# Kernel optimization log

Hardware: AMD Instinct MI355X
Metric: run time of the kernel (lower is better)

Reference implementation:

```python
import jax, jax.numpy as jnp
import numpy as np

N_NODES = 150000  # n_users + m_items
NUM_LAYERS = 3


def setup_inputs() -> dict:
    key = jax.random.key(0)
    k1, k2 = jax.random.split(key)
    x = jax.random.normal(k1, (N_NODES, 64), dtype=jnp.float32) * 0.1
    edge_index = jax.random.randint(k2, (2, 4800000), 0, N_NODES, dtype=jnp.int64)
    return {"x": x, "edge_index": edge_index}


def _lightgcn_propagate(x, row, col, deg_inv_sqrt):
    # message: norm * x[row], aggregated into col (sum)
    norm = deg_inv_sqrt[row] * deg_inv_sqrt[col]  # [E]
    msg = x[row] * norm[:, None]                   # [E, D]
    return jax.ops.segment_sum(msg, col, num_segments=x.shape[0])


def reference(x, edge_index):
    row, col = edge_index[0], edge_index[1]
    # symmetric GCN normalization: deg from destination nodes
    ones = jnp.ones(row.shape, dtype=x.dtype)
    deg = jax.ops.segment_sum(ones, col, num_segments=x.shape[0])
    deg_inv_sqrt = jnp.where(deg > 0, jax.lax.rsqrt(jnp.maximum(deg, 1.0)), 0.0)

    alpha = 1.0 / (1.0 + NUM_LAYERS)
    out = jnp.zeros_like(x)
    h = x
    for _ in range(NUM_LAYERS):
        h = _lightgcn_propagate(h, row, col, deg_inv_sqrt)
        out = out + alpha * h
    return out
```

## Files before the change

### kernel.cpp

```cpp
#include <hip/hip_runtime.h>
#include <hip/hip_fp16.h>
#include <math.h>

#define N_NODES 150000
#define D 64
#define NEDGE 4800000
#define NUM_LAYERS 3

#define BSHIFT 8
#define NBUCKET ((N_NODES + 255) >> 8)
#define NBPAD 768
#define BINTILE 8192
#define NBIN_BLOCKS ((NEDGE + BINTILE - 1) / BINTILE)
#define SCAP 9216

typedef float v2f __attribute__((ext_vector_type(2)));

__global__ void hist_bucket(const int4* __restrict__ col4, int* __restrict__ bcount) {
    __shared__ int h[NBUCKET];
    for (int i = threadIdx.x; i < NBUCKET; i += blockDim.x) h[i] = 0;
    __syncthreads();
    int i = blockIdx.x * blockDim.x + threadIdx.x;
    int stride = gridDim.x * blockDim.x;
    for (int e = i; e < NEDGE / 4; e += stride) {
        int4 c = col4[e];
        atomicAdd(&h[c.x >> BSHIFT], 1);
        atomicAdd(&h[c.y >> BSHIFT], 1);
        atomicAdd(&h[c.z >> BSHIFT], 1);
        atomicAdd(&h[c.w >> BSHIFT], 1);
    }
    __syncthreads();
    for (int b = threadIdx.x; b < NBUCKET; b += blockDim.x)
        if (h[b]) atomicAdd(&bcount[b], h[b]);
}

__global__ void scan_buckets(const int* __restrict__ bcount, int* __restrict__ bbase,
                             int* __restrict__ bcur16, int* __restrict__ off) {
    __shared__ int tsum[256];
    int t = threadIdx.x;
    int loc[3];
    int s = 0;
#pragma unroll
    for (int k = 0; k < 3; k++) {
        int idx = t * 3 + k;
        int x = (idx < NBUCKET) ? bcount[idx] : 0;
        loc[k] = x;
        s += x;
    }
    tsum[t] = s;
    __syncthreads();
    for (int ofs = 1; ofs < 256; ofs <<= 1) {
        int xv = (t >= ofs) ? tsum[t - ofs] : 0;
        __syncthreads();
        tsum[t] += xv;
        __syncthreads();
    }
    int run = (t > 0) ? tsum[t - 1] : 0;
#pragma unroll
    for (int k = 0; k < 3; k++) {
        int idx = t * 3 + k;
        if (idx < NBUCKET) bbase[idx] = run;
        bcur16[idx * 16] = run;
        run += loc[k];
    }
    if (t == 255) {
        bbase[NBUCKET] = NEDGE;
        off[N_NODES] = NEDGE;
    }
}

__global__ void __launch_bounds__(256) binpass2(const int* __restrict__ row,
                                                const int* __restrict__ col,
                                                int* __restrict__ bcur16,
                                                unsigned* __restrict__ bin) {
    __shared__ unsigned srec[BINTILE];
    __shared__ int hist[NBPAD];
    __shared__ int lscan[NBPAD];
    __shared__ int lcur[NBPAD];
    __shared__ int gbase[NBPAD];
    __shared__ int tsum[256];
    int t = threadIdx.x;
    int base = blockIdx.x * BINTILE;
    int n = NEDGE - base;
    if (n > BINTILE) n = BINTILE;
    for (int i = t; i < NBPAD; i += 256) hist[i] = 0;
    __syncthreads();
    for (int i = t; i < n; i += 256)
        atomicAdd(&hist[col[base + i] >> BSHIFT], 1);
    __syncthreads();
    int b0 = t * 3;
    int l0 = hist[b0], l1 = hist[b0 + 1], l2 = hist[b0 + 2];
    tsum[t] = l0 + l1 + l2;
    __syncthreads();
    for (int ofs = 1; ofs < 256; ofs <<= 1) {
        int xv = (t >= ofs) ? tsum[t - ofs] : 0;
        __syncthreads();
        tsum[t] += xv;
        __syncthreads();
    }
    int run = (t > 0) ? tsum[t - 1] : 0;
    lscan[b0] = run; lcur[b0] = run;
    lscan[b0 + 1] = run + l0; lcur[b0 + 1] = run + l0;
    lscan[b0 + 2] = run + l0 + l1; lcur[b0 + 2] = run + l0 + l1;
    gbase[b0]     = l0 ? atomicAdd(&bcur16[b0 * 16], l0) : 0;
    gbase[b0 + 1] = l1 ? atomicAdd(&bcur16[(b0 + 1) * 16], l1) : 0;
    gbase[b0 + 2] = l2 ? atomicAdd(&bcur16[(b0 + 2) * 16], l2) : 0;
    __syncthreads();
    for (int i = t; i < n; i += 256) {
        int c = col[base + i];
        int r = row[base + i];
        int b = c >> BSHIFT;
        int pos = atomicAdd(&lcur[b], 1);
        srec[pos] = (unsigned)r | ((unsigned)(c & 255) << 18);
    }
    __syncthreads();
#pragma unroll
    for (int k = 0; k < 3; k++) {
        int b = b0 + k;
        int s = lscan[b], e2 = lcur[b], gb = gbase[b];
        for (int j = s; j < e2; j++) bin[gb + (j - s)] = srec[j];
    }
}

__global__ void __launch_bounds__(256) sortpass2(const unsigned* __restrict__ bin,
                                                 const int* __restrict__ bbase,
                                                 float* __restrict__ dis,
                                                 int* __restrict__ off,
                                                 unsigned* __restrict__ ewf) {
    __shared__ unsigned srec[SCAP];
    __shared__ int hist[256];
    __shared__ int sc[256];
    __shared__ int ncur[256];
    int b = blockIdx.x, t = threadIdx.x;
    int s = bbase[b], e = bbase[b + 1];
    int len = e - s;
    int nst = len < SCAP ? len : SCAP;
    for (int i = t; i < nst; i += 256) srec[i] = bin[s + i];
    hist[t] = 0;
    __syncthreads();
    for (int i = t; i < nst; i += 256)
        atomicAdd(&hist[srec[i] >> 18], 1);
    for (int i = nst + t; i < len; i += 256)
        atomicAdd(&hist[bin[s + i] >> 18], 1);
    __syncthreads();
    int val = hist[t];
    sc[t] = val;
    __syncthreads();
    for (int ofs = 1; ofs < 256; ofs <<= 1) {
        int xv = (t >= ofs) ? sc[t - ofs] : 0;
        __syncthreads();
        sc[t] += xv;
        __syncthreads();
    }
    int ex = sc[t] - val;
    ncur[t] = ex;
    int node = (b << BSHIFT) + t;
    if (node < N_NODES) {
        dis[node] = (val > 0) ? (1.0f / sqrtf((float)val)) : 0.0f;
        off[node] = s + ex;
    }
    __syncthreads();
#pragma unroll
    for (int q = 0; q < 5; q++) {
        for (int i = t; i < nst; i += 256) {
            unsigned rec = srec[i];
            unsigned src = rec & 0x3FFFFu;
            if ((src >> 15) == (unsigned)q) {
                int c = (int)(rec >> 18);
                int pos = s + atomicAdd(&ncur[c], 1);
                ewf[pos] = src;
            }
        }
        __syncthreads();
    }
    for (int i = nst + t; i < len; i += 256) {
        unsigned rec = bin[s + i];
        int c = (int)(rec >> 18);
        int pos = s + atomicAdd(&ncur[c], 1);
        ewf[pos] = rec & 0x3FFFFu;
    }
}

__global__ void cvt_x(const float4* __restrict__ x4, uint2* __restrict__ xh) {
    int i = blockIdx.x * blockDim.x + threadIdx.x;
    if (i >= N_NODES * 16) return;
    float4 v = x4[i];
    __half2 a = __floats2half2_rn(v.x, v.y);
    __half2 b = __floats2half2_rn(v.z, v.w);
    uint2 r;
    r.x = *reinterpret_cast<unsigned*>(&a);
    r.y = *reinterpret_cast<unsigned*>(&b);
    xh[i] = r;
}

template <bool FINAL>
__global__ void layer8(const char* __restrict__ hbase, const int* __restrict__ off,
                       const unsigned* __restrict__ ewf, const float* __restrict__ dis,
                       char* __restrict__ hout, const char* __restrict__ hA,
                       const char* __restrict__ hB, float4* __restrict__ out4,
                       float alpha) {
    int wid = (blockIdx.x * blockDim.x + threadIdx.x) >> 6;
    if (wid >= N_NODES) return;
    unsigned lane = threadIdx.x & 63u;
    unsigned g = lane >> 3;
    unsigned sub16 = (lane & 7u) << 4;
    int s = off[wid], e = off[wid + 1];
    v2f acc[4];
#pragma unroll
    for (int k = 0; k < 4; k++) acc[k] = (v2f){0.f, 0.f};

    auto ACC = [&](uint4 v, float w) {
        v2f wv = {w, w};
        const __half2* p = reinterpret_cast<const __half2*>(&v);
#pragma unroll
        for (int k = 0; k < 4; k++) {
            float2 f = __half22float2(p[k]);
            v2f fv = {f.x, f.y};
            acc[k] += fv * wv;
        }
    };
    auto ROW = [&](unsigned r) {
        return *reinterpret_cast<const uint4*>(hbase + ((r << 7) | sub16));
    };

    int i = s + (int)g;
    for (; i + 24 < e; i += 32) {
        unsigned r0 = ewf[i], r1 = ewf[i + 8], r2 = ewf[i + 16], r3 = ewf[i + 24];
        float w0 = dis[r0], w1 = dis[r1], w2 = dis[r2], w3 = dis[r3];
        uint4 v0 = ROW(r0), v1 = ROW(r1), v2 = ROW(r2), v3 = ROW(r3);
        ACC(v0, w0); ACC(v1, w1); ACC(v2, w2); ACC(v3, w3);
    }
    for (; i < e; i += 8) {
        unsigned r = ewf[i];
        float w = dis[r];
        uint4 v = ROW(r);
        ACC(v, w);
    }
#pragma unroll
    for (int m = 8; m <= 32; m <<= 1)
#pragma unroll
        for (int k = 0; k < 4; k++) {
            acc[k].x += __shfl_xor(acc[k].x, m, 64);
            acc[k].y += __shfl_xor(acc[k].y, m, 64);
        }

    if (g != 0) return;
    float w = dis[wid];
    unsigned ro = ((unsigned)wid << 7) | sub16;
    if (FINAL) {
        uint4 a = *reinterpret_cast<const uint4*>(hA + ro);
        uint4 b = *reinterpret_cast<const uint4*>(hB + ro);
        const __half2* pa = reinterpret_cast<const __half2*>(&a);
        const __half2* pb = reinterpret_cast<const __half2*>(&b);
        float r[8];
#pragma unroll
        for (int k = 0; k < 4; k++) {
            float2 fa = __half22float2(pa[k]);
            float2 fb = __half22float2(pb[k]);
            r[2 * k]     = alpha * (fa.x + fb.x + w * acc[k].x);
            r[2 * k + 1] = alpha * (fa.y + fb.y + w * acc[k].y);
        }
        unsigned sub = (lane & 7u);
        out4[(size_t)wid * 16 + sub * 2]     = make_float4(r[0], r[1], r[2], r[3]);
        out4[(size_t)wid * 16 + sub * 2 + 1] = make_float4(r[4], r[5], r[6], r[7]);
    } else {
        __half2 q[4];
#pragma unroll
        for (int k = 0; k < 4; k++)
            q[k] = __floats2half2_rn(w * acc[k].x, w * acc[k].y);
        uint4 st;
        st.x = *reinterpret_cast<unsigned*>(&q[0]);
        st.y = *reinterpret_cast<unsigned*>(&q[1]);
        st.z = *reinterpret_cast<unsigned*>(&q[2]);
        st.w = *reinterpret_cast<unsigned*>(&q[3]);
        *reinterpret_cast<uint4*>(hout + ro) = st;
    }
}

extern "C" void kernel_launch(void* const* d_in, const int* in_sizes, int n_in,
                              void* d_out, int out_size, void* d_ws, size_t ws_size,
                              hipStream_t stream) {
    const float* x = (const float*)d_in[0];
    const int* edges = (const int*)d_in[1];
    const int* row = edges;
    const int* col = edges + NEDGE;
    float4* out4 = (float4*)d_out;

    char* ws = (char*)d_ws;
    size_t p = 0;
    auto alloc = [&](size_t bytes) {
        void* r = ws + p;
        p += (bytes + 255) & ~(size_t)255;
        return r;
    };
    int* bcount = (int*)alloc((size_t)NBUCKET * 4);
    int* bbase = (int*)alloc((size_t)(NBUCKET + 1) * 4);
    int* bcur16 = (int*)alloc((size_t)NBPAD * 16 * 4);
    float* dis = (float*)alloc((size_t)N_NODES * 4);
    int* off = (int*)alloc((size_t)(N_NODES + 1) * 4);
    unsigned* ewf = (unsigned*)alloc((size_t)NEDGE * 4);
    char* xh = (char*)alloc((size_t)N_NODES * D * 2);
    char* region = (char*)alloc((size_t)N_NODES * D * 2);
    unsigned* bin = (unsigned*)region;
    char* hA = region;
    char* hB = (char*)alloc((size_t)N_NODES * D * 2);

    hipMemsetAsync(bcount, 0, (size_t)NBUCKET * 4, stream);
    cvt_x<<<(N_NODES * 16 + 255) / 256, 256, 0, stream>>>((const float4*)x, (uint2*)xh);
    hist_bucket<<<512, 256, 0, stream>>>((const int4*)col, bcount);
    scan_buckets<<<1, 256, 0, stream>>>(bcount, bbase, bcur16, off);
    binpass2<<<NBIN_BLOCKS, 256, 0, stream>>>(row, col, bcur16, bin);
    sortpass2<<<NBUCKET, 256, 0, stream>>>(bin, bbase, dis, off, ewf);

    const float alpha = 1.0f / (1.0f + NUM_LAYERS);
    int grid = (N_NODES * 64 + 255) / 256;
    layer8<false><<<grid, 256, 0, stream>>>(xh, off, ewf, dis,
                                            hA, nullptr, nullptr, nullptr, alpha);
    layer8<false><<<grid, 256, 0, stream>>>(hA, off, ewf, dis,
                                            hB, nullptr, nullptr, nullptr, alpha);
    layer8<true><<<grid, 256, 0, stream>>>(hB, off, ewf, dis,
                                           nullptr, hA, hB, out4, alpha);
}
```

Measured before the change: 407.7 us.

## Prescale features by source degree norm to drop per-edge dis gathers

Stores g = dis * h instead of h, so each layer accumulates plain neighbor rows and applies dis^2 per destination node, removing the random per-edge gather of dis[src]. The final layer recovers h from g by dividing by dis. The sort pass also drops its five-pass source-range ordering of the shared-memory edges, which had been there to improve gather locality. This trades a per-edge dependent load for extra fp16 rounding of scaled values and possible loss of the locality-friendly edge order.

After: 385.2 us. 1.06x faster.

```diff
diff --git a/kernel.cpp b/kernel.cpp
--- a/kernel.cpp
+++ b/kernel.cpp
@@ -160,18 +160,11 @@
         off[node] = s + ex;
     }
     __syncthreads();
-#pragma unroll
-    for (int q = 0; q < 5; q++) {
-        for (int i = t; i < nst; i += 256) {
-            unsigned rec = srec[i];
-            unsigned src = rec & 0x3FFFFu;
-            if ((src >> 15) == (unsigned)q) {
-                int c = (int)(rec >> 18);
-                int pos = s + atomicAdd(&ncur[c], 1);
-                ewf[pos] = src;
-            }
-        }
-        __syncthreads();
+    for (int i = t; i < nst; i += 256) {
+        unsigned rec = srec[i];
+        int c = (int)(rec >> 18);
+        int pos = s + atomicAdd(&ncur[c], 1);
+        ewf[pos] = rec & 0x3FFFFu;
     }
     for (int i = nst + t; i < len; i += 256) {
         unsigned rec = bin[s + i];
@@ -181,16 +174,18 @@
     }
 }
 
-__global__ void cvt_x(const float4* __restrict__ x4, uint2* __restrict__ xh) {
+__global__ void cvt_g0(const float4* __restrict__ x4, const float* __restrict__ dis,
+                       uint2* __restrict__ g0) {
     int i = blockIdx.x * blockDim.x + threadIdx.x;
     if (i >= N_NODES * 16) return;
+    float w = dis[i >> 4];
     float4 v = x4[i];
-    __half2 a = __floats2half2_rn(v.x, v.y);
-    __half2 b = __floats2half2_rn(v.z, v.w);
+    __half2 a = __floats2half2_rn(w * v.x, w * v.y);
+    __half2 b = __floats2half2_rn(w * v.z, w * v.w);
     uint2 r;
     r.x = *reinterpret_cast<unsigned*>(&a);
     r.y = *reinterpret_cast<unsigned*>(&b);
-    xh[i] = r;
+    g0[i] = r;
 }
 
 template <bool FINAL>
@@ -209,14 +204,12 @@
 #pragma unroll
     for (int k = 0; k < 4; k++) acc[k] = (v2f){0.f, 0.f};
 
-    auto ACC = [&](uint4 v, float w) {
-        v2f wv = {w, w};
+    auto ACC = [&](uint4 v) {
         const __half2* p = reinterpret_cast<const __half2*>(&v);
 #pragma unroll
         for (int k = 0; k < 4; k++) {
             float2 f = __half22float2(p[k]);
-            v2f fv = {f.x, f.y};
-            acc[k] += fv * wv;
+            acc[k] += (v2f){f.x, f.y};
         }
     };
     auto ROW = [&](unsigned r) {
@@ -226,16 +219,11 @@
     int i = s + (int)g;
     for (; i + 24 < e; i += 32) {
         unsigned r0 = ewf[i], r1 = ewf[i + 8], r2 = ewf[i + 16], r3 = ewf[i + 24];
-        float w0 = dis[r0], w1 = dis[r1], w2 = dis[r2], w3 = dis[r3];
         uint4 v0 = ROW(r0), v1 = ROW(r1), v2 = ROW(r2), v3 = ROW(r3);
-        ACC(v0, w0); ACC(v1, w1); ACC(v2, w2); ACC(v3, w3);
-    }
-    for (; i < e; i += 8) {
-        unsigned r = ewf[i];
-        float w = dis[r];
-        uint4 v = ROW(r);
-        ACC(v, w);
-    }
+        ACC(v0); ACC(v1); ACC(v2); ACC(v3);
+    }
+    for (; i < e; i += 8) ACC(ROW(ewf[i]));
+
 #pragma unroll
     for (int m = 8; m <= 32; m <<= 1)
 #pragma unroll
@@ -248,6 +236,7 @@
     float w = dis[wid];
     unsigned ro = ((unsigned)wid << 7) | sub16;
     if (FINAL) {
+        float inv = (w > 0.f) ? 1.0f / w : 0.f;
         uint4 a = *reinterpret_cast<const uint4*>(hA + ro);
         uint4 b = *reinterpret_cast<const uint4*>(hB + ro);
         const __half2* pa = reinterpret_cast<const __half2*>(&a);
@@ -257,17 +246,18 @@
         for (int k = 0; k < 4; k++) {
             float2 fa = __half22float2(pa[k]);
             float2 fb = __half22float2(pb[k]);
-            r[2 * k]     = alpha * (fa.x + fb.x + w * acc[k].x);
-            r[2 * k + 1] = alpha * (fa.y + fb.y + w * acc[k].y);
+            r[2 * k]     = alpha * (inv * (fa.x + fb.x) + w * acc[k].x);
+            r[2 * k + 1] = alpha * (inv * (fa.y + fb.y) + w * acc[k].y);
         }
         unsigned sub = (lane & 7u);
         out4[(size_t)wid * 16 + sub * 2]     = make_float4(r[0], r[1], r[2], r[3]);
         out4[(size_t)wid * 16 + sub * 2 + 1] = make_float4(r[4], r[5], r[6], r[7]);
     } else {
+        float w2 = w * w;
         __half2 q[4];
 #pragma unroll
         for (int k = 0; k < 4; k++)
-            q[k] = __floats2half2_rn(w * acc[k].x, w * acc[k].y);
+            q[k] = __floats2half2_rn(w2 * acc[k].x, w2 * acc[k].y);
         uint4 st;
         st.x = *reinterpret_cast<unsigned*>(&q[0]);
         st.y = *reinterpret_cast<unsigned*>(&q[1]);
@@ -299,25 +289,26 @@
     float* dis = (float*)alloc((size_t)N_NODES * 4);
     int* off = (int*)alloc((size_t)(N_NODES + 1) * 4);
     unsigned* ewf = (unsigned*)alloc((size_t)NEDGE * 4);
-    char* xh = (char*)alloc((size_t)N_NODES * D * 2);
+    char* g0 = (char*)alloc((size_t)N_NODES * D * 2);
     char* region = (char*)alloc((size_t)N_NODES * D * 2);
     unsigned* bin = (unsigned*)region;
-    char* hA = region;
-    char* hB = (char*)alloc((size_t)N_NODES * D * 2);
+    char* g1 = region;
+    char* g2 = (char*)alloc((size_t)N_NODES * D * 2);
 
     hipMemsetAsync(bcount, 0, (size_t)NBUCKET * 4, stream);
-    cvt_x<<<(N_NODES * 16 + 255) / 256, 256, 0, stream>>>((const float4*)x, (uint2*)xh);
     hist_bucket<<<512, 256, 0, stream>>>((const int4*)col, bcount);
     scan_buckets<<<1, 256, 0, stream>>>(bcount, bbase, bcur16, off);
     binpass2<<<NBIN_BLOCKS, 256, 0, stream>>>(row, col, bcur16, bin);
     sortpass2<<<NBUCKET, 256, 0, stream>>>(bin, bbase, dis, off, ewf);
+    cvt_g0<<<(N_NODES * 16 + 255) / 256, 256, 0, stream>>>((const float4*)x, dis,
+                                                           (uint2*)g0);
 
     const float alpha = 1.0f / (1.0f + NUM_LAYERS);
     int grid = (N_NODES * 64 + 255) / 256;
-    layer8<false><<<grid, 256, 0, stream>>>(xh, off, ewf, dis,
-                                            hA, nullptr, nullptr, nullptr, alpha);
-    layer8<false><<<grid, 256, 0, stream>>>(hA, off, ewf, dis,
-                                            hB, nullptr, nullptr, nullptr, alpha);
-    layer8<true><<<grid, 256, 0, stream>>>(hB, off, ewf, dis,
-                                           nullptr, hA, hB, out4, alpha);
-}
+    layer8<false><<<grid, 256, 0, stream>>>(g0, off, ewf, dis,
+                                            g1, nullptr, nullptr, nullptr, alpha);
+    layer8<false><<<grid, 256, 0, stream>>>(g1, off, ewf, dis,
+                                            g2, nullptr, nullptr, nullptr, alpha);
+    layer8<true><<<grid, 256, 0, stream>>>(g2, off, ewf, dis,
+                                           nullptr, g1, g2, out4, alpha);
+}
```
